# Kernel optimization log

Measured on AMD Instinct MI355X. Metric: run time of the kernel, lower is better.

## Reference

```python
import jax, jax.numpy as jnp
import numpy as np

B, C, N = 8, 128, 4096  # (batch, channels=dim, time); F = N//2+1 = 2049 (odd)


def setup_inputs() -> dict:
    key = jax.random.key(0)
    ks = jax.random.split(key, 7)
    s = 1.0 / np.sqrt(C)
    return {
        "x_in": jax.random.normal(ks[0], (B, C, N), dtype=jnp.float32),
        "W_K": jax.random.normal(ks[1], (C, C), dtype=jnp.float32) * s,
        "b_K": jax.random.normal(ks[2], (C,), dtype=jnp.float32) * s,
        "W_V": jax.random.normal(ks[3], (C, C), dtype=jnp.float32) * s,
        "b_V": jax.random.normal(ks[4], (C,), dtype=jnp.float32) * s,
        "w_high": jax.random.normal(ks[5], (C, 2), dtype=jnp.float32) * 0.02,
        "threshold_param": jax.random.uniform(ks[6], (1,), dtype=jnp.float32) * 0.5,
    }


def reference(x_in, W_K, b_K, W_V, b_V, w_high, threshold_param):
    x = jnp.transpose(x_in, (0, 2, 1)).astype(jnp.float32)  # (B, N, C)
    _, n, c = x.shape
    x_fft = jnp.fft.rfft(x, axis=1, norm="ortho")            # (B, F, C) complex64
    K = jnp.fft.rfft(x @ W_K.T + b_K, axis=1, norm="ortho")  # (B, F, C)
    V = jnp.fft.rfft(x @ W_V.T + b_V, axis=1, norm="ortho")  # (B, F, C)
    scale = c ** (-0.5)
    # complex attention scores (no conjugation, matching torch.matmul(Q, K^T))
    attn = jnp.einsum("bfc,bgc->bfg", x_fft, K) * scale      # (B, F, F) complex
    attn = jax.nn.softmax(jnp.abs(attn), axis=-1)            # real softmax of |scores|
    context = jnp.einsum("bfg,bgc->bfc", attn.astype(x_fft.dtype), V)
    # adaptive high-frequency mask
    energy = jnp.sum(jnp.abs(x_fft) ** 2, axis=-1)           # (B, F)
    median_energy = jnp.median(energy, axis=1, keepdims=True)
    normalized = energy / (median_energy + 1e-6)
    threshold = jnp.quantile(normalized, threshold_param[0])  # global quantile
    mask = (normalized > threshold)[:, :, None]               # (B, F, 1)
    w_hi = w_high[:, 0] + 1j * w_high[:, 1]                   # (C,) complex
    context = context + jnp.where(mask, x_fft, 0.0) * w_hi
    out = jnp.fft.irfft(context, n=n, axis=1, norm="ortho")  # (B, N, C) float32
    return jnp.transpose(out, (0, 2, 1))                      # (B, C, N)
```

## Files before the change

kernel.cpp:

```cpp
#include <hip/hip_runtime.h>
#include <math.h>

#define NB 8
#define NC 128
#define NT 4096
#define NF 2049
#define FP 2176

typedef __bf16 bf16;
typedef __bf16 bf16x2 __attribute__((ext_vector_type(2)));
typedef __bf16 bf16x8 __attribute__((ext_vector_type(8)));
typedef float f32x4 __attribute__((ext_vector_type(4)));
typedef unsigned int uint32x4 __attribute__((ext_vector_type(4)));

__device__ __forceinline__ void async16(const bf16* g, bf16* l) {
    __builtin_amdgcn_global_load_lds(
        (const __attribute__((address_space(1))) void*)g,
        (__attribute__((address_space(3))) void*)l, 16, 0, 0);
}

__device__ __forceinline__ bf16x8 derive_b2(bf16x8 v) {
    uint32x4 u = __builtin_bit_cast(uint32x4, v);
#pragma unroll
    for (int i = 0; i < 4; ++i)
        u[i] = (((u[i] >> 16) | (u[i] << 16)) ^ 0x00008000u);
    return __builtin_bit_cast(bf16x8, u);
}

__global__ __launch_bounds__(256) void twiddle_kernel(float2* __restrict__ tw) {
    int k = blockIdx.x * 256 + threadIdx.x;
    if (k < 2048) {
        float ang = (float)M_PI * (float)k * (1.0f / 2048.0f);
        float sw, cw;
        __sincosf(ang, &sw, &cw);
        tw[k] = make_float2(cw, -sw);
    }
}

__device__ __forceinline__ void fft4096(float2* buf, const float2* __restrict__ tw) {
    int mult = 2048;
    for (int half = 1; half < NT; half <<= 1) {
        __syncthreads();
        for (int t = threadIdx.x; t < NT / 2; t += 256) {
            int pos = t & (half - 1);
            int i = 2 * t - pos;
            int j = i + half;
            float2 w = tw[pos * mult];
            float cw = w.x, sw = w.y;
            float2 u = buf[i], v = buf[j];
            float vr = v.x * cw - v.y * sw;
            float vi = v.x * sw + v.y * cw;
            buf[i] = make_float2(u.x + vr, u.y + vi);
            buf[j] = make_float2(u.x - vr, u.y - vi);
        }
        mult >>= 1;
    }
    __syncthreads();
}

__global__ __launch_bounds__(256) void fft_fwd_kernel(const float* __restrict__ x_in,
                                                      const float2* __restrict__ tw,
                                                      float2* __restrict__ Xc) {
    __shared__ float2 buf[NT];
    int bc = blockIdx.x;
    const float* xrow = x_in + (size_t)bc * NT;
    for (int i = threadIdx.x; i < NT; i += 256) {
        int r = __brev((unsigned)i) >> 20;
        buf[r] = make_float2(xrow[i], 0.0f);
    }
    fft4096(buf, tw);
    const float inv = 1.0f / 64.0f;
    float2* orow = Xc + (size_t)bc * NF;
    for (int f = threadIdx.x; f < NF; f += 256) {
        float2 v = buf[f];
        orow[f] = make_float2(v.x * inv, v.y * inv);
    }
}

__global__ __launch_bounds__(256) void xt_kernel(const float2* __restrict__ Xc,
                                                 float2* __restrict__ Xf2,
                                                 bf16* __restrict__ Xb) {
    __shared__ float2 tile[64][65];
    int blk = blockIdx.x;
    int b = blk / 68;
    int t2 = blk % 68;
    int c0 = (t2 / 34) * 64;
    int f0 = (t2 % 34) * 64;
    int t = threadIdx.x;
    int fl = t & 63, cc = t >> 6;
#pragma unroll
    for (int cb = 0; cb < 16; ++cb) {
        int cl = cb * 4 + cc;
        int f = f0 + fl;
        float2 v = make_float2(0.f, 0.f);
        if (f < NF) v = Xc[((size_t)b * NC + c0 + cl) * NF + f];
        tile[fl][cl] = v;
    }
    __syncthreads();
    int chl = t & 63, ww = t >> 6;
#pragma unroll
    for (int wb = 0; wb < 16; ++wb) {
        int fl2 = wb * 4 + ww;
        int f = f0 + fl2;
        float2 v = tile[fl2][chl];
        if (f < NF) Xf2[((size_t)b * NF + f) * 128 + c0 + chl] = v;
        bf16x2 p;
        p[0] = (bf16)v.x; p[1] = (bf16)v.y;
        *(bf16x2*)&Xb[((size_t)b * FP + f) * 256 + 2 * (c0 + chl)] = p;
    }
}

__global__ __launch_bounds__(256) void wpack_kernel(const float* __restrict__ W_K,
                                                    const float* __restrict__ W_V,
                                                    bf16* __restrict__ Wk1,
                                                    bf16* __restrict__ Av) {
    int idx = blockIdx.x * 256 + threadIdx.x;
    if (idx < 256 * 256) {
        int n = idx >> 8, k = idx & 255;
        int c = k >> 1;
        int j = n >> 1;
        float v = 0.f;
        if (!(n & 1) && !(k & 1)) v = W_K[j * NC + c];
        else if ((n & 1) && (k & 1)) v = -W_K[j * NC + c];
        Wk1[idx] = (bf16)v;
        float v2 = 0.f;
        if (!(n & 1) && !(k & 1)) v2 = W_V[j * NC + c];
        else if ((n & 1) && (k & 1)) v2 = W_V[j * NC + c];
        Av[idx] = (bf16)v2;
    }
}

__global__ __launch_bounds__(256, 2) void kvgemm_kernel(const bf16* __restrict__ Xb,
                                                        const bf16* __restrict__ Wk1,
                                                        bf16* __restrict__ K1) {
    __shared__ __align__(16) bf16 As[128 * 64];
    __shared__ __align__(16) bf16 Bs[128 * 64];
    int blk = blockIdx.x;
    int b = blk & 7;
    int t2 = blk >> 3;
    int g0 = (t2 >> 1) * 128;
    int n0 = (t2 & 1) * 128;
    int tid = threadIdx.x;
    int wave = tid >> 6, lane = tid & 63;
    int m = lane & 15, quad = lane >> 4;
    int row_off = (wave & 1) * 64, col_off = (wave >> 1) * 64;
    int lrow = lane >> 3;
    int cswz = (lane & 7) ^ lrow;
    int mk = m & 7;

    f32x4 acc[4][4] = {};
    const bf16* Abase = Xb + ((size_t)b * FP + g0) * 256;
    const bf16* Bbase = Wk1 + (size_t)n0 * 256;

    for (int kk = 0; kk < 256; kk += 64) {
        __syncthreads();
#pragma unroll
        for (int t = 0; t < 4; ++t) {
            int r0 = wave * 32 + t * 8;
            async16(Abase + (size_t)(r0 + lrow) * 256 + kk + cswz * 8, As + r0 * 64);
            async16(Bbase + (size_t)(r0 + lrow) * 256 + kk + cswz * 8, Bs + r0 * 64);
        }
        __syncthreads();
#pragma unroll
        for (int k2 = 0; k2 < 64; k2 += 32) {
            bf16x8 a[4], bb[4];
            int pos = (((k2 >> 3) + quad) ^ mk) << 3;
#pragma unroll
            for (int i = 0; i < 4; ++i) a[i] = *(const bf16x8*)&As[(row_off + i * 16 + m) * 64 + pos];
#pragma unroll
            for (int j = 0; j < 4; ++j) bb[j] = *(const bf16x8*)&Bs[(col_off + j * 16 + m) * 64 + pos];
#pragma unroll
            for (int i = 0; i < 4; ++i)
#pragma unroll
                for (int j = 0; j < 4; ++j)
                    acc[i][j] = __builtin_amdgcn_mfma_f32_16x16x32_bf16(a[i], bb[j], acc[i][j], 0, 0, 0);
        }
    }
#pragma unroll
    for (int i = 0; i < 4; ++i)
#pragma unroll
        for (int j = 0; j < 4; ++j)
#pragma unroll
            for (int r = 0; r < 4; ++r) {
                int row = g0 + row_off + i * 16 + quad * 4 + r;
                int col = n0 + col_off + j * 16 + m;
                K1[((size_t)b * FP + row) * 256 + col] = (bf16)acc[i][j][r];
            }
}

__global__ __launch_bounds__(256, 2) void vtgemm_kernel(const bf16* __restrict__ Av,
                                                        const bf16* __restrict__ Xb,
                                                        bf16* __restrict__ Vt) {
    __shared__ __align__(16) bf16 As[128 * 64];
    __shared__ __align__(16) bf16 Bs[128 * 64];
    int blk = blockIdx.x;
    int b = blk & 7;
    int t2 = blk >> 3;
    int g0 = (t2 >> 1) * 128;
    int n0 = (t2 & 1) * 128;
    int tid = threadIdx.x;
    int wave = tid >> 6, lane = tid & 63;
    int m = lane & 15, quad = lane >> 4;
    int row_off = (wave & 1) * 64, col_off = (wave >> 1) * 64;
    int lrow = lane >> 3;
    int cswz = (lane & 7) ^ lrow;
    int mk = m & 7;

    f32x4 acc[4][4] = {};
    const bf16* Abase = Av + (size_t)n0 * 256;
    const bf16* Bbase = Xb + ((size_t)b * FP + g0) * 256;

    for (int kk = 0; kk < 256; kk += 64) {
        __syncthreads();
#pragma unroll
        for (int t = 0; t < 4; ++t) {
            int r0 = wave * 32 + t * 8;
            async16(Abase + (size_t)(r0 + lrow) * 256 + kk + cswz * 8, As + r0 * 64);
            async16(Bbase + (size_t)(r0 + lrow) * 256 + kk + cswz * 8, Bs + r0 * 64);
        }
        __syncthreads();
#pragma unroll
        for (int k2 = 0; k2 < 64; k2 += 32) {
            bf16x8 a[4], bb[4];
            int pos = (((k2 >> 3) + quad) ^ mk) << 3;
#pragma unroll
            for (int i = 0; i < 4; ++i) a[i] = *(const bf16x8*)&As[(row_off + i * 16 + m) * 64 + pos];
#pragma unroll
            for (int j = 0; j < 4; ++j) bb[j] = *(const bf16x8*)&Bs[(col_off + j * 16 + m) * 64 + pos];
#pragma unroll
            for (int i = 0; i < 4; ++i)
#pragma unroll
                for (int j = 0; j < 4; ++j)
                    acc[i][j] = __builtin_amdgcn_mfma_f32_16x16x32_bf16(a[i], bb[j], acc[i][j], 0, 0, 0);
        }
    }
#pragma unroll
    for (int i = 0; i < 4; ++i)
#pragma unroll
        for (int j = 0; j < 4; ++j)
#pragma unroll
            for (int r = 0; r < 4; ++r) {
                int row = n0 + row_off + i * 16 + quad * 4 + r;
                int col = g0 + col_off + j * 16 + m;
                Vt[((size_t)b * 256 + row) * FP + col] = (bf16)acc[i][j][r];
            }
}

__global__ __launch_bounds__(128) void biasfix_kernel(const float* __restrict__ b_K,
                                                      const float* __restrict__ b_V,
                                                      bf16* __restrict__ K1,
                                                      bf16* __restrict__ Vt) {
    int b = blockIdx.x;
    int j = threadIdx.x;
    float bk = 64.0f * b_K[j], bv = 64.0f * b_V[j];
    size_t o = (size_t)b * FP * 256;
    K1[o + 2 * j] = (bf16)((float)K1[o + 2 * j] + bk);
    size_t ov = ((size_t)b * 256 + 2 * j) * FP;
    Vt[ov] = (bf16)((float)Vt[ov] + bv);
}

__global__ __launch_bounds__(256) void energy_kernel(const float* __restrict__ Xf,
                                                     float* __restrict__ energy) {
    int idx = blockIdx.x * 256 + threadIdx.x;
    if (idx >= NB * NF) return;
    const float4* row = (const float4*)(Xf + (size_t)idx * 2 * NC);
    float e = 0.f;
    for (int i = 0; i < 64; ++i) {
        float4 v = row[i];
        e += v.x * v.x + v.y * v.y + v.z * v.z + v.w * v.w;
    }
    energy[idx] = e;
}

__global__ __launch_bounds__(256) void median_kernel(const float* __restrict__ energy,
                                                     float* __restrict__ med) {
    int blk = blockIdx.x;
    int b = blk / 9, chunk = blk % 9;
    __shared__ __align__(16) float e[2052];
    for (int i = threadIdx.x; i < 2052; i += 256)
        e[i] = (i < NF) ? energy[b * NF + i] : INFINITY;
    __syncthreads();
    int i = chunk * 256 + threadIdx.x;
    float ei = (i < NF) ? e[i] : 0.f;
    int rank = 0;
#pragma unroll 4
    for (int j4 = 0; j4 < 513; ++j4) {
        float4 v = ((const float4*)e)[j4];
        int j = j4 * 4;
        rank += (v.x < ei) || (v.x == ei && j + 0 < i);
        rank += (v.y < ei) || (v.y == ei && j + 1 < i);
        rank += (v.z < ei) || (v.z == ei && j + 2 < i);
        rank += (v.w < ei) || (v.w == ei && j + 3 < i);
    }
    if (i < NF && rank == 1024) med[b] = ei;
}

__global__ __launch_bounds__(256) void norm_kernel(const float* __restrict__ energy,
                                                   const float* __restrict__ med,
                                                   float* __restrict__ nrm) {
    int idx = blockIdx.x * 256 + threadIdx.x;
    if (idx >= NB * NF) return;
    int b = idx / NF;
    nrm[idx] = energy[idx] / (med[b] + 1e-6f);
}

__global__ __launch_bounds__(256) void rankpart_kernel(const float* __restrict__ nrm,
                                                       int* __restrict__ rankpart) {
    const int n = NB * NF;
    int cb = blockIdx.x / 17;
    int chunk = blockIdx.x % 17;
    __shared__ __align__(16) float cdata[1024];
    int base = chunk * 1024;
    for (int t = threadIdx.x; t < 1024; t += 256)
        cdata[t] = (base + t < n) ? nrm[base + t] : INFINITY;
    __syncthreads();
    int i = cb * 256 + threadIdx.x;
    if (i >= n) return;
    float ei = nrm[i];
    int rank = 0;
#pragma unroll 8
    for (int t4 = 0; t4 < 256; ++t4) {
        float4 v = ((const float4*)cdata)[t4];
        int j = base + t4 * 4;
        rank += (v.x < ei) || (v.x == ei && j + 0 < i);
        rank += (v.y < ei) || (v.y == ei && j + 1 < i);
        rank += (v.z < ei) || (v.z == ei && j + 2 < i);
        rank += (v.w < ei) || (v.w == ei && j + 3 < i);
    }
    rankpart[(size_t)i * 17 + chunk] = rank;
}

__global__ __launch_bounds__(256) void rankreduce_kernel(const int* __restrict__ rankpart,
                                                         const float* __restrict__ nrm,
                                                         const float* __restrict__ q,
                                                         float* __restrict__ vk) {
    const int n = NB * NF;
    int i = blockIdx.x * 256 + threadIdx.x;
    if (i >= n) return;
    int rank = 0;
    const int* rp = rankpart + (size_t)i * 17;
#pragma unroll
    for (int c = 0; c < 17; ++c) rank += rp[c];
    double pos = (double)q[0] * (double)(n - 1);
    int k0 = (int)floor(pos);
    int k1 = min(k0 + 1, n - 1);
    if (rank == k0) vk[0] = nrm[i];
    if (rank == k1) vk[1] = nrm[i];
}

__global__ void thresh_kernel(const float* __restrict__ vk,
                              const float* __restrict__ q,
                              float* __restrict__ thr) {
    if (threadIdx.x == 0 && blockIdx.x == 0) {
        const int n = NB * NF;
        double pos = (double)q[0] * (double)(n - 1);
        double k0 = floor(pos);
        double frac = pos - k0;
        thr[0] = (float)((double)vk[0] + ((double)vk[1] - (double)vk[0]) * frac);
    }
}

__global__ __launch_bounds__(256, 3) void score_kernel(const bf16* __restrict__ Xb,
                                                       const bf16* __restrict__ K1,
                                                       bf16* __restrict__ S) {
    __shared__ __align__(16) char smem[24576];
    bf16* As  = (bf16*)smem;
    bf16* B1s = (bf16*)(smem + 16384);
    int blk = blockIdx.x;
    int b = blk & 7;
    int t2 = blk >> 3;
    int f0 = (t2 / 34) * 128;
    int g0 = (t2 % 34) * 64;
    int tid = threadIdx.x;
    int wave = tid >> 6, lane = tid & 63;
    int m = lane & 15, quad = lane >> 4;
    int row_off = (wave & 1) * 64, col_off = (wave >> 1) * 32;

    f32x4 accRe[4][2] = {};
    f32x4 accIm[4][2] = {};
    const bf16* Abase = Xb + ((size_t)b * FP + f0) * 256;
    const bf16* Kbase = K1 + ((size_t)b * FP + g0) * 256;
    int lrow = lane >> 3;
    int cswz = (lane & 7) ^ lrow;
    int mk = m & 7;

    for (int kk = 0; kk < 256; kk += 64) {
        __syncthreads();
#pragma unroll
        for (int t = 0; t < 4; ++t) {
            int r0 = wave * 32 + t * 8;
            async16(Abase + (size_t)(r0 + lrow) * 256 + kk + cswz * 8, As + r0 * 64);
        }
#pragma unroll
        for (int t = 0; t < 2; ++t) {
            int r0 = wave * 16 + t * 8;
            async16(Kbase + (size_t)(r0 + lrow) * 256 + kk + cswz * 8, B1s + r0 * 64);
        }
        __syncthreads();
#pragma unroll
        for (int k2 = 0; k2 < 64; k2 += 32) {
            bf16x8 a[4], b1[2], b2[2];
            int pos = (((k2 >> 3) + quad) ^ mk) << 3;
#pragma unroll
            for (int i = 0; i < 4; ++i)
                a[i] = *(const bf16x8*)&As[(row_off + i * 16 + m) * 64 + pos];
#pragma unroll
            for (int j = 0; j < 2; ++j) {
                b1[j] = *(const bf16x8*)&B1s[(col_off + j * 16 + m) * 64 + pos];
                b2[j] = derive_b2(b1[j]);
            }
#pragma unroll
            for (int i = 0; i < 4; ++i)
#pragma unroll
                for (int j = 0; j < 2; ++j) {
                    accRe[i][j] = __builtin_amdgcn_mfma_f32_16x16x32_bf16(a[i], b1[j], accRe[i][j], 0, 0, 0);
                    accIm[i][j] = __builtin_amdgcn_mfma_f32_16x16x32_bf16(a[i], b2[j], accIm[i][j], 0, 0, 0);
                }
        }
    }
    const float SCALE = 0.08838834764831845f;
    __syncthreads();
    bf16 (*Cs)[72] = (bf16(*)[72])smem;
#pragma unroll
    for (int i = 0; i < 4; ++i)
#pragma unroll
        for (int j = 0; j < 2; ++j)
#pragma unroll
            for (int r = 0; r < 4; ++r) {
                float re = accRe[i][j][r], im = accIm[i][j][r];
                Cs[row_off + i * 16 + quad * 4 + r][col_off + j * 16 + m] =
                    (bf16)(sqrtf(re * re + im * im) * SCALE);
            }
    __syncthreads();
    bf16* Sb = S + (size_t)b * FP * FP;
    int row = tid >> 1, half = tid & 1;
    const bf16* src = &Cs[row][half * 32];
    bf16* dst = Sb + (size_t)(f0 + row) * FP + g0 + half * 32;
#pragma unroll
    for (int u = 0; u < 4; ++u)
        *(bf16x8*)&dst[u * 8] = *(const bf16x8*)&src[u * 8];
}

__global__ __launch_bounds__(256) void softmax_kernel(bf16* __restrict__ S) {
    int bf = blockIdx.x;
    int b = bf / NF, f = bf % NF;
    bf16* row = S + ((size_t)b * FP + f) * FP;
    int t = threadIdx.x;
    __shared__ float red[256];
    bf16x8 raw = *(const bf16x8*)&row[t * 8];
    float tail = (t == 0) ? (float)row[2048] : -1e30f;
    float v[8];
    float mx = tail;
#pragma unroll
    for (int u = 0; u < 8; ++u) { v[u] = (float)raw[u]; mx = fmaxf(mx, v[u]); }
    red[t] = mx;
    __syncthreads();
    for (int s = 128; s > 0; s >>= 1) {
        if (t < s) red[t] = fmaxf(red[t], red[t + s]);
        __syncthreads();
    }
    float mval = red[0];
    __syncthreads();
    float sum = 0.f;
#pragma unroll
    for (int u = 0; u < 8; ++u) { v[u] = __expf(v[u] - mval); sum += v[u]; }
    float tex = 0.f;
    if (t == 0) { tex = __expf(tail - mval); sum += tex; }
    red[t] = sum;
    __syncthreads();
    for (int s = 128; s > 0; s >>= 1) {
        if (t < s) red[t] += red[t + s];
        __syncthreads();
    }
    float inv = 1.f / red[0];
    bf16x8 outv;
#pragma unroll
    for (int u = 0; u < 8; ++u) outv[u] = (bf16)(v[u] * inv);
    *(bf16x8*)&row[t * 8] = outv;
    if (t == 0) row[2048] = (bf16)(tex * inv);
    if (t < FP - NF) row[NF + t] = (bf16)0.f;
}

__global__ __launch_bounds__(256) void context_kernel(const bf16* __restrict__ P,
                                                      const bf16* __restrict__ Vt,
                                                      float* __restrict__ Ctx) {
    __shared__ __align__(16) bf16 Ps[64 * 64];
    __shared__ __align__(16) bf16 Vs[256 * 64];
    int blk = blockIdx.x;
    int b = blk & 7;
    int f0 = (blk >> 3) * 64;
    int tid = threadIdx.x;
    int wave = tid >> 6, lane = tid & 63;
    int m = lane & 15, quad = lane >> 4;
    int col_off = wave * 64;
    int lrow = lane >> 3;
    int cswz = (lane & 7) ^ lrow;
    int mk = m & 7;

    f32x4 acc[4][4] = {};
    const bf16* Pbase = P + ((size_t)b * FP + f0) * FP;
    const bf16* Vbase = Vt + (size_t)b * 256 * FP;

    for (int kk = 0; kk < FP; kk += 64) {
        __syncthreads();
#pragma unroll
        for (int t = 0; t < 2; ++t) {
            int r0 = wave * 16 + t * 8;
            async16(Pbase + (size_t)(r0 + lrow) * FP + kk + cswz * 8, Ps + r0 * 64);
        }
#pragma unroll
        for (int t = 0; t < 8; ++t) {
            int r0 = wave * 64 + t * 8;
            async16(Vbase + (size_t)(r0 + lrow) * FP + kk + cswz * 8, Vs + r0 * 64);
        }
        __syncthreads();
#pragma unroll
        for (int k2 = 0; k2 < 64; k2 += 32) {
            bf16x8 a[4], bb[4];
            int pos = (((k2 >> 3) + quad) ^ mk) << 3;
#pragma unroll
            for (int i = 0; i < 4; ++i) a[i] = *(const bf16x8*)&Ps[(i * 16 + m) * 64 + pos];
#pragma unroll
            for (int j = 0; j < 4; ++j) bb[j] = *(const bf16x8*)&Vs[(col_off + j * 16 + m) * 64 + pos];
#pragma unroll
            for (int i = 0; i < 4; ++i)
#pragma unroll
                for (int j = 0; j < 4; ++j)
                    acc[i][j] = __builtin_amdgcn_mfma_f32_16x16x32_bf16(a[i], bb[j], acc[i][j], 0, 0, 0);
        }
    }
#pragma unroll
    for (int i = 0; i < 4; ++i)
#pragma unroll
        for (int j = 0; j < 4; ++j)
#pragma unroll
            for (int r = 0; r < 4; ++r) {
                int row = f0 + i * 16 + quad * 4 + r;
                int col = col_off + j * 16 + m;
                if (row < NF) Ctx[((size_t)b * NF + row) * 256 + col] = acc[i][j][r];
            }
}

__global__ __launch_bounds__(256) void ctxt_kernel(const float2* __restrict__ Ctx2,
                                                   const float2* __restrict__ Xf2,
                                                   const float* __restrict__ nrm,
                                                   const float* __restrict__ thr,
                                                   const float* __restrict__ w_high,
                                                   float* __restrict__ Ctxt) {
    __shared__ float2 tile[64][33];
    int blk = blockIdx.x;
    int b = blk / 132;
    int t2 = blk % 132;
    int cp0 = (t2 / 33) * 32;
    int f0 = (t2 % 33) * 64;
    int t = threadIdx.x;
    float thrv = thr[0];
    int cpl = t & 31, rr = t >> 5;
#pragma unroll
    for (int rb = 0; rb < 8; ++rb) {
        int fl = rb * 8 + rr;
        int f = f0 + fl;
        float2 v = make_float2(0.f, 0.f);
        if (f < NF) {
            size_t idx = ((size_t)b * NF + f) * 128 + cp0 + cpl;
            v = Ctx2[idx];
            if (nrm[b * NF + f] > thrv) {
                float2 x = Xf2[idx];
                int c = cp0 + cpl;
                float wr = w_high[2 * c], wi = w_high[2 * c + 1];
                v.x += x.x * wr - x.y * wi;
                v.y += x.x * wi + x.y * wr;
            }
        }
        tile[fl][cpl] = v;
    }
    __syncthreads();
    int fl = t & 63, ww = t >> 6;
#pragma unroll
    for (int wb = 0; wb < 16; ++wb) {
        int chl = wb * 4 + ww;
        int f = f0 + fl;
        if (f < NF) {
            float2 v = tile[fl][chl >> 1];
            Ctxt[((size_t)b * 256 + 2 * cp0 + chl) * NF + f] = (chl & 1) ? v.y : v.x;
        }
    }
}

__global__ __launch_bounds__(256) void fft_inv_kernel(const float* __restrict__ Ctxt,
                                                      const float2* __restrict__ tw,
                                                      float* __restrict__ out) {
    __shared__ float2 buf[NT];
    int bc = blockIdx.x, b = bc >> 7, c = bc & 127;
    const float* base = Ctxt + ((size_t)b * 256 + 2 * c) * NF;
    const float* basei = base + NF;
    for (int f = threadIdx.x; f < NT; f += 256) {
        float re, im;
        if (f <= NT / 2) {
            re = base[f];
            im = -basei[f];
        } else {
            int g = NT - f;
            re = base[g];
            im = basei[g];
        }
        int r = __brev((unsigned)f) >> 20;
        buf[r] = make_float2(re, im);
    }
    fft4096(buf, tw);
    float* orow = out + (size_t)bc * NT;
    const float inv = 1.0f / 64.0f;
    for (int n = threadIdx.x; n < NT; n += 256) orow[n] = buf[n].x * inv;
}

extern "C" void kernel_launch(void* const* d_in, const int* in_sizes, int n_in,
                              void* d_out, int out_size, void* d_ws, size_t ws_size,
                              hipStream_t stream) {
    const float* x_in = (const float*)d_in[0];
    const float* W_K = (const float*)d_in[1];
    const float* b_K = (const float*)d_in[2];
    const float* W_V = (const float*)d_in[3];
    const float* b_V = (const float*)d_in[4];
    const float* w_high = (const float*)d_in[5];
    const float* qpar = (const float*)d_in[6];
    float* out = (float*)d_out;

    char* w = (char*)d_ws;
    const size_t SPECB = (size_t)NB * NF * 256 * 4;
    float* Xf = (float*)w;            w += SPECB;
    float* Ctx = (float*)w;           w += SPECB;
    float* energy = (float*)w;        w += (size_t)NB * NF * 4;
    float* med = (float*)w;           w += 64;
    float* nrm = (float*)w;           w += (size_t)NB * NF * 4;
    float* vk = (float*)w;            w += 64;
    float* thr = (float*)w;           w += 64;
    w = (char*)(((uintptr_t)w + 255) & ~(uintptr_t)255);
    float2* tw = (float2*)w;          w += (size_t)2048 * 8;
    int* rankpart = (int*)w;          w += (size_t)16640 * 17 * 4;
    w = (char*)(((uintptr_t)w + 255) & ~(uintptr_t)255);
    bf16* S = (bf16*)w;               w += (size_t)NB * FP * FP * 2;
    bf16* Xb = (bf16*)w;              w += (size_t)NB * FP * 256 * 2;
    bf16* K1 = (bf16*)w;              w += (size_t)NB * FP * 256 * 2;
    bf16* Vt = (bf16*)w;              w += (size_t)NB * 256 * FP * 2;
    bf16* Wk1 = (bf16*)w;             w += (size_t)256 * 256 * 2;
    bf16* Av = (bf16*)w;              w += (size_t)256 * 256 * 2;
    float2* Xc = (float2*)S;
    float* Ctxt = (float*)Xb;

    twiddle_kernel<<<8, 256, 0, stream>>>(tw);
    fft_fwd_kernel<<<NB * NC, 256, 0, stream>>>(x_in, tw, Xc);
    xt_kernel<<<NB * 2 * 34, 256, 0, stream>>>(Xc, (float2*)Xf, Xb);
    wpack_kernel<<<256, 256, 0, stream>>>(W_K, W_V, Wk1, Av);
    kvgemm_kernel<<<NB * 17 * 2, 256, 0, stream>>>(Xb, Wk1, K1);
    vtgemm_kernel<<<NB * 17 * 2, 256, 0, stream>>>(Av, Xb, Vt);
    biasfix_kernel<<<NB, 128, 0, stream>>>(b_K, b_V, K1, Vt);
    energy_kernel<<<(NB * NF + 255) / 256, 256, 0, stream>>>(Xf, energy);
    median_kernel<<<NB * 9, 256, 0, stream>>>(energy, med);
    norm_kernel<<<(NB * NF + 255) / 256, 256, 0, stream>>>(energy, med, nrm);
    rankpart_kernel<<<65 * 17, 256, 0, stream>>>(nrm, rankpart);
    rankreduce_kernel<<<65, 256, 0, stream>>>(rankpart, nrm, qpar, vk);
    thresh_kernel<<<1, 64, 0, stream>>>(vk, qpar, thr);
    score_kernel<<<NB * 17 * 34, 256, 0, stream>>>(Xb, K1, S);
    softmax_kernel<<<NB * NF, 256, 0, stream>>>(S);
    context_kernel<<<NB * 33, 256, 0, stream>>>(S, Vt, Ctx);
    ctxt_kernel<<<NB * 4 * 33, 256, 0, stream>>>((const float2*)Ctx, (const float2*)Xf,
                                                 nrm, thr, w_high, Ctxt);
    fft_inv_kernel<<<NB * NC, 256, 0, stream>>>(Ctxt, tw, out);
}
```

Measured before the change: 434.8 us.

## Fuse softmax into score and context kernels; use radix-4 FFT

The standalone softmax pass is removed. The score kernel now also emits per-tile row maxima and exp-sums, a small rowstat kernel combines them into a per-row log-normaliser, and the context kernel applies exp(s - c) on the fly while staging probability tiles into shared memory. This avoids a full read and write of the large bf16 score matrix, at the cost of extra exp work inside the GEMM and possible reliance on the padded columns already being harmless. The context kernel also uses 32-row tiles for more blocks, and the 4096-point FFT switches from radix-2 to radix-4 with digit-reversed input, halving the number of barrier-separated stages.

```diff
diff --git a/kernel.cpp b/kernel.cpp
--- a/kernel.cpp
+++ b/kernel.cpp
@@ -25,6 +25,10 @@
     for (int i = 0; i < 4; ++i)
         u[i] = (((u[i] >> 16) | (u[i] << 16)) ^ 0x00008000u);
     return __builtin_bit_cast(bf16x8, u);
+}
+
+__device__ __forceinline__ float2 cmulf(float2 a, float2 b) {
+    return make_float2(a.x * b.x - a.y * b.y, a.x * b.y + a.y * b.x);
 }
 
 __global__ __launch_bounds__(256) void twiddle_kernel(float2* __restrict__ tw) {
@@ -38,24 +42,39 @@
 }
 
 __device__ __forceinline__ void fft4096(float2* buf, const float2* __restrict__ tw) {
-    int mult = 2048;
-    for (int half = 1; half < NT; half <<= 1) {
-        __syncthreads();
-        for (int t = threadIdx.x; t < NT / 2; t += 256) {
-            int pos = t & (half - 1);
-            int i = 2 * t - pos;
-            int j = i + half;
-            float2 w = tw[pos * mult];
-            float cw = w.x, sw = w.y;
-            float2 u = buf[i], v = buf[j];
-            float vr = v.x * cw - v.y * sw;
-            float vi = v.x * sw + v.y * cw;
-            buf[i] = make_float2(u.x + vr, u.y + vi);
-            buf[j] = make_float2(u.x - vr, u.y - vi);
-        }
-        mult >>= 1;
-    }
-    __syncthreads();
+    int sh = 0;
+#pragma unroll
+    for (int s6 = 0; s6 < 6; ++s6) {
+        int L = 1 << sh;
+        __syncthreads();
+        for (int t = threadIdx.x; t < 1024; t += 256) {
+            int pos = t & (L - 1);
+            int base = ((t >> sh) << (sh + 2)) + pos;
+            int k1 = pos << (10 - sh);
+            float2 w1 = tw[k1];
+            float2 w2 = tw[2 * k1];
+            float2 w3 = cmulf(w1, w2);
+            float2 x0 = buf[base];
+            float2 x1 = cmulf(buf[base + L], w1);
+            float2 x2 = cmulf(buf[base + 2 * L], w2);
+            float2 x3 = cmulf(buf[base + 3 * L], w3);
+            float2 b0 = make_float2(x0.x + x2.x, x0.y + x2.y);
+            float2 b1 = make_float2(x0.x - x2.x, x0.y - x2.y);
+            float2 b2 = make_float2(x1.x + x3.x, x1.y + x3.y);
+            float2 b3 = make_float2(x1.x - x3.x, x1.y - x3.y);
+            buf[base]         = make_float2(b0.x + b2.x, b0.y + b2.y);
+            buf[base + L]     = make_float2(b1.x + b3.y, b1.y - b3.x);
+            buf[base + 2 * L] = make_float2(b0.x - b2.x, b0.y - b2.y);
+            buf[base + 3 * L] = make_float2(b1.x - b3.y, b1.y + b3.x);
+        }
+        sh += 2;
+    }
+    __syncthreads();
+}
+
+__device__ __forceinline__ unsigned dr4(unsigned i) {
+    unsigned r = __brev(i) >> 20;
+    return ((r & 0x555u) << 1) | ((r & 0xAAAu) >> 1);
 }
 
 __global__ __launch_bounds__(256) void fft_fwd_kernel(const float* __restrict__ x_in,
@@ -64,10 +83,8 @@
     __shared__ float2 buf[NT];
     int bc = blockIdx.x;
     const float* xrow = x_in + (size_t)bc * NT;
-    for (int i = threadIdx.x; i < NT; i += 256) {
-        int r = __brev((unsigned)i) >> 20;
-        buf[r] = make_float2(xrow[i], 0.0f);
-    }
+    for (int i = threadIdx.x; i < NT; i += 256)
+        buf[dr4((unsigned)i)] = make_float2(xrow[i], 0.0f);
     fft4096(buf, tw);
     const float inv = 1.0f / 64.0f;
     float2* orow = Xc + (size_t)bc * NF;
@@ -362,7 +379,9 @@
 
 __global__ __launch_bounds__(256, 3) void score_kernel(const bf16* __restrict__ Xb,
                                                        const bf16* __restrict__ K1,
-                                                       bf16* __restrict__ S) {
+                                                       bf16* __restrict__ S,
+                                                       float* __restrict__ Mpart,
+                                                       float* __restrict__ Lpart) {
     __shared__ __align__(16) char smem[24576];
     bf16* As  = (bf16*)smem;
     bf16* B1s = (bf16*)(smem + 16384);
@@ -370,7 +389,8 @@
     int b = blk & 7;
     int t2 = blk >> 3;
     int f0 = (t2 / 34) * 128;
-    int g0 = (t2 % 34) * 64;
+    int gblk = t2 % 34;
+    int g0 = gblk * 64;
     int tid = threadIdx.x;
     int wave = tid >> 6, lane = tid & 63;
     int m = lane & 15, quad = lane >> 4;
@@ -432,63 +452,67 @@
                     (bf16)(sqrtf(re * re + im * im) * SCALE);
             }
     __syncthreads();
+    float* mred = (float*)(smem + 18432);
+    float* lred = (float*)(smem + 19456);
     bf16* Sb = S + (size_t)b * FP * FP;
     int row = tid >> 1, half = tid & 1;
     const bf16* src = &Cs[row][half * 32];
     bf16* dst = Sb + (size_t)(f0 + row) * FP + g0 + half * 32;
-#pragma unroll
-    for (int u = 0; u < 4; ++u)
-        *(bf16x8*)&dst[u * 8] = *(const bf16x8*)&src[u * 8];
-}
-
-__global__ __launch_bounds__(256) void softmax_kernel(bf16* __restrict__ S) {
-    int bf = blockIdx.x;
-    int b = bf / NF, f = bf % NF;
-    bf16* row = S + ((size_t)b * FP + f) * FP;
-    int t = threadIdx.x;
-    __shared__ float red[256];
-    bf16x8 raw = *(const bf16x8*)&row[t * 8];
-    float tail = (t == 0) ? (float)row[2048] : -1e30f;
-    float v[8];
-    float mx = tail;
-#pragma unroll
-    for (int u = 0; u < 8; ++u) { v[u] = (float)raw[u]; mx = fmaxf(mx, v[u]); }
-    red[t] = mx;
-    __syncthreads();
-    for (int s = 128; s > 0; s >>= 1) {
-        if (t < s) red[t] = fmaxf(red[t], red[t + s]);
-        __syncthreads();
-    }
-    float mval = red[0];
-    __syncthreads();
-    float sum = 0.f;
-#pragma unroll
-    for (int u = 0; u < 8; ++u) { v[u] = __expf(v[u] - mval); sum += v[u]; }
-    float tex = 0.f;
-    if (t == 0) { tex = __expf(tail - mval); sum += tex; }
-    red[t] = sum;
-    __syncthreads();
-    for (int s = 128; s > 0; s >>= 1) {
-        if (t < s) red[t] += red[t + s];
-        __syncthreads();
-    }
-    float inv = 1.f / red[0];
-    bf16x8 outv;
-#pragma unroll
-    for (int u = 0; u < 8; ++u) outv[u] = (bf16)(v[u] * inv);
-    *(bf16x8*)&row[t * 8] = outv;
-    if (t == 0) row[2048] = (bf16)(tex * inv);
-    if (t < FP - NF) row[NF + t] = (bf16)0.f;
-}
-
-__global__ __launch_bounds__(256) void context_kernel(const bf16* __restrict__ P,
+    int gbase = g0 + half * 32;
+    float lmax = -1e30f;
+#pragma unroll
+    for (int u = 0; u < 4; ++u) {
+        bf16x8 v8 = *(const bf16x8*)&src[u * 8];
+        *(bf16x8*)&dst[u * 8] = v8;
+#pragma unroll
+        for (int e = 0; e < 8; ++e)
+            if (gbase + u * 8 + e <= 2048) lmax = fmaxf(lmax, (float)v8[e]);
+    }
+    mred[tid] = lmax;
+    __syncthreads();
+    float rmax = fmaxf(mred[row * 2], mred[row * 2 + 1]);
+    float lsum = 0.f;
+#pragma unroll
+    for (int u = 0; u < 4; ++u) {
+        bf16x8 v8 = *(const bf16x8*)&src[u * 8];
+#pragma unroll
+        for (int e = 0; e < 8; ++e)
+            if (gbase + u * 8 + e <= 2048) lsum += __expf((float)v8[e] - rmax);
+    }
+    lred[tid] = lsum;
+    __syncthreads();
+    if (half == 0) {
+        size_t ro = ((size_t)b * FP + f0 + row) * 34 + gblk;
+        Mpart[ro] = rmax;
+        Lpart[ro] = lred[row * 2] + lred[row * 2 + 1];
+    }
+}
+
+__global__ __launch_bounds__(256) void rowstat_kernel(const float* __restrict__ Mpart,
+                                                      const float* __restrict__ Lpart,
+                                                      float* __restrict__ Crow) {
+    int row = blockIdx.x * 256 + threadIdx.x;
+    if (row >= NB * FP) return;
+    const float* mp = Mpart + (size_t)row * 34;
+    const float* lp = Lpart + (size_t)row * 34;
+    float M = -1e30f;
+#pragma unroll
+    for (int i = 0; i < 34; ++i) M = fmaxf(M, mp[i]);
+    float L = 0.f;
+#pragma unroll
+    for (int i = 0; i < 34; ++i) L += lp[i] * __expf(mp[i] - M);
+    Crow[row] = M + __logf(L);
+}
+
+__global__ __launch_bounds__(256) void context_kernel(const bf16* __restrict__ Sg,
+                                                      const float* __restrict__ Crow,
                                                       const bf16* __restrict__ Vt,
                                                       float* __restrict__ Ctx) {
-    __shared__ __align__(16) bf16 Ps[64 * 64];
+    __shared__ __align__(16) bf16 Ps[32 * 64];
     __shared__ __align__(16) bf16 Vs[256 * 64];
     int blk = blockIdx.x;
     int b = blk & 7;
-    int f0 = (blk >> 3) * 64;
+    int f0 = (blk >> 3) * 32;
     int tid = threadIdx.x;
     int wave = tid >> 6, lane = tid & 63;
     int m = lane & 15, quad = lane >> 4;
@@ -497,40 +521,44 @@
     int cswz = (lane & 7) ^ lrow;
     int mk = m & 7;
 
-    f32x4 acc[4][4] = {};
-    const bf16* Pbase = P + ((size_t)b * FP + f0) * FP;
+    f32x4 acc[2][4] = {};
+    int prow = wave * 8 + lrow;
+    const bf16* Prow = Sg + ((size_t)b * FP + f0 + prow) * FP;
+    float cst = Crow[(size_t)b * FP + f0 + prow];
     const bf16* Vbase = Vt + (size_t)b * 256 * FP;
 
     for (int kk = 0; kk < FP; kk += 64) {
         __syncthreads();
-#pragma unroll
-        for (int t = 0; t < 2; ++t) {
-            int r0 = wave * 16 + t * 8;
-            async16(Pbase + (size_t)(r0 + lrow) * FP + kk + cswz * 8, Ps + r0 * 64);
-        }
 #pragma unroll
         for (int t = 0; t < 8; ++t) {
             int r0 = wave * 64 + t * 8;
             async16(Vbase + (size_t)(r0 + lrow) * FP + kk + cswz * 8, Vs + r0 * 64);
         }
+        {
+            bf16x8 s8 = *(const bf16x8*)&Prow[kk + cswz * 8];
+            bf16x8 p8;
+#pragma unroll
+            for (int e = 0; e < 8; ++e) p8[e] = (bf16)__expf((float)s8[e] - cst);
+            *(bf16x8*)&Ps[prow * 64 + (lane & 7) * 8] = p8;
+        }
         __syncthreads();
 #pragma unroll
         for (int k2 = 0; k2 < 64; k2 += 32) {
-            bf16x8 a[4], bb[4];
+            bf16x8 a[2], bb[4];
             int pos = (((k2 >> 3) + quad) ^ mk) << 3;
 #pragma unroll
-            for (int i = 0; i < 4; ++i) a[i] = *(const bf16x8*)&Ps[(i * 16 + m) * 64 + pos];
+            for (int i = 0; i < 2; ++i) a[i] = *(const bf16x8*)&Ps[(i * 16 + m) * 64 + pos];
 #pragma unroll
             for (int j = 0; j < 4; ++j) bb[j] = *(const bf16x8*)&Vs[(col_off + j * 16 + m) * 64 + pos];
 #pragma unroll
-            for (int i = 0; i < 4; ++i)
+            for (int i = 0; i < 2; ++i)
 #pragma unroll
                 for (int j = 0; j < 4; ++j)
                     acc[i][j] = __builtin_amdgcn_mfma_f32_16x16x32_bf16(a[i], bb[j], acc[i][j], 0, 0, 0);
         }
     }
 #pragma unroll
-    for (int i = 0; i < 4; ++i)
+    for (int i = 0; i < 2; ++i)
 #pragma unroll
         for (int j = 0; j < 4; ++j)
 #pragma unroll
@@ -604,8 +632,7 @@
             re = base[g];
             im = basei[g];
         }
-        int r = __brev((unsigned)f) >> 20;
-        buf[r] = make_float2(re, im);
+        buf[dr4((unsigned)f)] = make_float2(re, im);
     }
     fft4096(buf, tw);
     float* orow = out + (size_t)bc * NT;
@@ -638,6 +665,10 @@
     float2* tw = (float2*)w;          w += (size_t)2048 * 8;
     int* rankpart = (int*)w;          w += (size_t)16640 * 17 * 4;
     w = (char*)(((uintptr_t)w + 255) & ~(uintptr_t)255);
+    float* Mpart = (float*)w;         w += (size_t)NB * FP * 34 * 4;
+    float* Lpart = (float*)w;         w += (size_t)NB * FP * 34 * 4;
+    float* Crow = (float*)w;          w += (size_t)NB * FP * 4;
+    w = (char*)(((uintptr_t)w + 255) & ~(uintptr_t)255);
     bf16* S = (bf16*)w;               w += (size_t)NB * FP * FP * 2;
     bf16* Xb = (bf16*)w;              w += (size_t)NB * FP * 256 * 2;
     bf16* K1 = (bf16*)w;              w += (size_t)NB * FP * 256 * 2;
@@ -660,9 +691,9 @@
     rankpart_kernel<<<65 * 17, 256, 0, stream>>>(nrm, rankpart);
     rankreduce_kernel<<<65, 256, 0, stream>>>(rankpart, nrm, qpar, vk);
     thresh_kernel<<<1, 64, 0, stream>>>(vk, qpar, thr);
-    score_kernel<<<NB * 17 * 34, 256, 0, stream>>>(Xb, K1, S);
-    softmax_kernel<<<NB * NF, 256, 0, stream>>>(S);
-    context_kernel<<<NB * 33, 256, 0, stream>>>(S, Vt, Ctx);
+    score_kernel<<<NB * 17 * 34, 256, 0, stream>>>(Xb, K1, S, Mpart, Lpart);
+    rowstat_kernel<<<(NB * FP + 255) / 256, 256, 0, stream>>>(Mpart, Lpart, Crow);
+    context_kernel<<<NB * 65, 256, 0, stream>>>(S, Crow, Vt, Ctx);
     ctxt_kernel<<<NB * 4 * 33, 256, 0, stream>>>((const float2*)Ctx, (const float2*)Xf,
                                                  nrm, thr, w_high, Ctxt);
     fft_inv_kernel<<<NB * NC, 256, 0, stream>>>(Ctxt, tw, out);
```

New measurement: 409.8 us. -5.7%, faster.
